# Optimization experiments

Hardware: AMD Instinct MI355X
Metric: run time of the kernel (lower is better)

## Reference

```python
import jax, jax.numpy as jnp
import numpy as np

ALPHA = 0.2  # LeakyReLU negative slope
N_NODES = 50000
N_EDGES = 800000
IN_F = 128
OUT_F = 64


def setup_inputs() -> dict:
    key = jax.random.key(0)
    k1, k2, k3, k4 = jax.random.split(key, 4)
    x = jax.random.normal(k1, (N_NODES, IN_F), dtype=jnp.float32)
    edge_index = jax.random.randint(k2, (2, N_EDGES), 0, N_NODES, dtype=jnp.int64)
    # xavier_uniform-ish scales
    W = jax.random.uniform(k3, (IN_F, OUT_F), dtype=jnp.float32,
                           minval=-1.0, maxval=1.0) * (1.414 * np.sqrt(6.0 / (IN_F + OUT_F)))
    a = jax.random.uniform(k4, (2 * OUT_F, 1), dtype=jnp.float32,
                           minval=-1.0, maxval=1.0) * (1.414 * np.sqrt(6.0 / (2 * OUT_F + 1)))
    return {"x": x, "edge_index": edge_index, "W": W, "a": a}


def reference(x, edge_index, W, a):
    Wh = x @ W                               # [N, F_out]
    src = edge_index[0]
    dst = edge_index[1]
    Wh_src = Wh[src]                         # [E, F_out] gather
    Wh_dst = Wh[dst]                         # [E, F_out] gather
    # concat([Wh_src, Wh_dst]) @ a == Wh_src @ a_top + Wh_dst @ a_bot
    F_out = Wh.shape[1]
    a_top = a[:F_out, 0]
    a_bot = a[F_out:, 0]
    e = jax.nn.leaky_relu(Wh_src @ a_top + Wh_dst @ a_bot, negative_slope=ALPHA)  # [E]
    # NOTE: original normalizes softmax over ALL edges (dim=0), not per node.
    attention = jax.nn.softmax(e)            # [E]
    # dropout skipped (eval mode, deterministic reference)
    msgs = Wh_dst * attention[:, None]       # [E, F_out]
    h_prime = jax.ops.segment_sum(msgs, src, num_segments=Wh.shape[0])  # scatter-add
    return jax.nn.elu(h_prime)
```

## Files before the change

### kernel.cpp

```cpp
#include <hip/hip_runtime.h>
#include <math.h>

#define N_NODES 50000
#define N_EDGES 800000
#define IN_F 128
#define OUT_F 64
#define LRELU_ALPHA 0.2f

#define NPB 128
#define NBUCK ((N_NODES + NPB - 1) / NPB)
#define EPT 8
#define NBT ((N_EDGES / EPT + 255) / 256)
#define CHUNK 2048

typedef __attribute__((ext_vector_type(8))) short bf16x8;
typedef __attribute__((ext_vector_type(4))) float f32x4;

__device__ inline float wred_max(float v) {
#pragma unroll
    for (int o = 32; o > 0; o >>= 1) v = fmaxf(v, __shfl_down(v, o, 64));
    return v;
}
__device__ inline float wred_sum(float v) {
#pragma unroll
    for (int o = 32; o > 0; o >>= 1) v += __shfl_down(v, o, 64);
    return v;
}

__device__ inline unsigned bf16r(float f) {
    unsigned u = __float_as_uint(f);
    u += 0x7fffu + ((u >> 16) & 1u);
    return u >> 16;
}

__global__ __launch_bounds__(128) void k_proj(const float* __restrict__ W,
                                              const float* __restrict__ a,
                                              float* __restrict__ wt,
                                              float* __restrict__ wb,
                                              unsigned short* __restrict__ Wtb) {
    int k = threadIdx.x;
    float s = 0.0f, t = 0.0f;
#pragma unroll
    for (int c4 = 0; c4 < 64; c4 += 4) {
        float4 wv = *reinterpret_cast<const float4*>(W + k * 64 + c4);
        float4 at = *reinterpret_cast<const float4*>(a + c4);
        float4 ab = *reinterpret_cast<const float4*>(a + 64 + c4);
        s = fmaf(wv.w, at.w, fmaf(wv.z, at.z, fmaf(wv.y, at.y, fmaf(wv.x, at.x, s))));
        t = fmaf(wv.w, ab.w, fmaf(wv.z, ab.z, fmaf(wv.y, ab.y, fmaf(wv.x, ab.x, t))));
        Wtb[(c4 + 0) * 128 + k] = (unsigned short)bf16r(wv.x);
        Wtb[(c4 + 1) * 128 + k] = (unsigned short)bf16r(wv.y);
        Wtb[(c4 + 2) * 128 + k] = (unsigned short)bf16r(wv.z);
        Wtb[(c4 + 3) * 128 + k] = (unsigned short)bf16r(wv.w);
    }
    wt[k] = s;
    wb[k] = t;
}

__global__ __launch_bounds__(256, 4) void k_wh(const float* __restrict__ x,
                                               const unsigned short* __restrict__ Wtb,
                                               const float* __restrict__ wt,
                                               const float* __restrict__ wb,
                                               const int* __restrict__ src,
                                               unsigned short* __restrict__ Whb,
                                               float* __restrict__ sv,
                                               float* __restrict__ tv,
                                               int* __restrict__ bcnt) {
    __shared__ unsigned short xb[64 * 128];
    __shared__ unsigned short wtl[64 * 128];
    __shared__ int hc[NBUCK];

    const int tid = threadIdx.x;
    const int row0 = blockIdx.x * 64;

    for (int i = tid; i < NBUCK; i += 256) hc[i] = 0;

    for (int ci = tid; ci < 1024; ci += 256) {
        int c = ci >> 4, kb = ci & 15;
        int4 v = *reinterpret_cast<const int4*>(Wtb + ci * 8);
        *reinterpret_cast<int4*>(&wtl[c * 128 + (kb ^ (c & 15)) * 8]) = v;
    }

    const int cc = (tid & 31) << 2;
    float4 wt4 = *reinterpret_cast<const float4*>(wt + cc);
    float4 wb4 = *reinterpret_cast<const float4*>(wb + cc);
    float ps[8], pt[8];
#pragma unroll
    for (int it = 0; it < 8; ++it) {
        int i = tid + it * 256;
        int rl = i >> 5;
        int r = row0 + rl;
        float4 v = make_float4(0.f, 0.f, 0.f, 0.f);
        if (r < N_NODES) v = *reinterpret_cast<const float4*>(x + (size_t)r * IN_F + cc);
        ps[it] = fmaf(v.w, wt4.w, fmaf(v.z, wt4.z, fmaf(v.y, wt4.y, v.x * wt4.x)));
        pt[it] = fmaf(v.w, wb4.w, fmaf(v.z, wb4.z, fmaf(v.y, wb4.y, v.x * wb4.x)));
        int kb = cc >> 3;
        uint2 pk;
        pk.x = bf16r(v.x) | (bf16r(v.y) << 16);
        pk.y = bf16r(v.z) | (bf16r(v.w) << 16);
        *reinterpret_cast<uint2*>(
            &xb[rl * 128 + (kb ^ (rl & 15)) * 8 + ((cc >> 2) & 1) * 4]) = pk;
    }

    {
        int j0 = blockIdx.x * 1024 + tid * 4;
        if (j0 < N_EDGES) {
            int4 s4 = *reinterpret_cast<const int4*>(src + j0);
            atomicAdd(&hc[s4.x >> 7], 1);
            atomicAdd(&hc[s4.y >> 7], 1);
            atomicAdd(&hc[s4.z >> 7], 1);
            atomicAdd(&hc[s4.w >> 7], 1);
        }
    }
    __syncthreads();

    const int l = tid & 63, w = tid >> 6;
    const int rloc0 = w * 16;
    const int arow = rloc0 + (l & 15);
    const int kgrp = l >> 4;
    f32x4 acc[4] = {f32x4{0,0,0,0}, f32x4{0,0,0,0}, f32x4{0,0,0,0}, f32x4{0,0,0,0}};
#pragma unroll
    for (int t = 0; t < 4; ++t) {
        int kb = t * 4 + kgrp;
        bf16x8 af = *reinterpret_cast<const bf16x8*>(
            &xb[arow * 128 + (kb ^ (arow & 15)) * 8]);
#pragma unroll
        for (int ct = 0; ct < 4; ++ct) {
            int brow = ct * 16 + (l & 15);
            bf16x8 bfr = *reinterpret_cast<const bf16x8*>(
                &wtl[brow * 128 + (kb ^ (brow & 15)) * 8]);
            acc[ct] = __builtin_amdgcn_mfma_f32_16x16x32_bf16(af, bfr, acc[ct], 0, 0, 0);
        }
    }

#pragma unroll
    for (int ct = 0; ct < 4; ++ct) {
#pragma unroll
        for (int i = 0; i < 4; ++i) {
            int r = row0 + rloc0 + (l >> 4) * 4 + i;
            if (r < N_NODES)
                Whb[(size_t)r * OUT_F + ct * 16 + (l & 15)] =
                    (unsigned short)bf16r(acc[ct][i]);
        }
    }

#pragma unroll
    for (int it = 0; it < 8; ++it) {
        float s = ps[it], t2 = pt[it];
#pragma unroll
        for (int o = 1; o < 32; o <<= 1) {
            s += __shfl_xor(s, o, 64);
            t2 += __shfl_xor(t2, o, 64);
        }
        int r = row0 + (tid >> 5) + it * 8;
        if ((tid & 31) == 0 && r < N_NODES) { sv[r] = s; tv[r] = t2; }
    }

    __syncthreads();
    for (int i = tid; i < NBUCK; i += 256) {
        int v = hc[i];
        if (v) atomicAdd(&bcnt[i], v);
    }
}

__global__ __launch_bounds__(512) void k_bscan(const int* __restrict__ bcnt,
                                               int* __restrict__ bbase,
                                               int* __restrict__ cursor) {
    __shared__ int s[512];
    int t = threadIdx.x;
    int c = (t < NBUCK) ? bcnt[t] : 0;
    s[t] = c;
    __syncthreads();
#pragma unroll
    for (int o = 1; o < 512; o <<= 1) {
        int v = (t >= o) ? s[t - o] : 0;
        __syncthreads();
        s[t] += v;
        __syncthreads();
    }
    if (t < NBUCK) {
        int ex = s[t] - c;
        bbase[t] = ex;
        cursor[t] = ex;
    }
    if (t == 0) bbase[NBUCK] = N_EDGES;
}

__global__ __launch_bounds__(256) void k_binscatter(const int* __restrict__ src,
                                                    const int* __restrict__ dst,
                                                    const float* __restrict__ sv,
                                                    const float* __restrict__ tv,
                                                    int* __restrict__ cursor,
                                                    int2* __restrict__ rec,
                                                    float* __restrict__ pmax,
                                                    float* __restrict__ psum) {
    __shared__ int lcnt[NBUCK];
    __shared__ int lbase[NBUCK];
    const int tid = threadIdx.x;
    for (int i = tid; i < NBUCK; i += 256) lcnt[i] = 0;
    __syncthreads();

    int t = blockIdx.x * 256 + tid;
    int j0 = t * EPT;
    bool ok = (j0 < N_EDGES);

    int s_[EPT], d_[EPT], rk[EPT];
    float v[EPT];
    float lmax = -INFINITY;
    if (ok) {
        int4 a4 = *reinterpret_cast<const int4*>(src + j0);
        int4 b4 = *reinterpret_cast<const int4*>(src + j0 + 4);
        int4 c4 = *reinterpret_cast<const int4*>(dst + j0);
        int4 e4 = *reinterpret_cast<const int4*>(dst + j0 + 4);
        s_[0] = a4.x; s_[1] = a4.y; s_[2] = a4.z; s_[3] = a4.w;
        s_[4] = b4.x; s_[5] = b4.y; s_[6] = b4.z; s_[7] = b4.w;
        d_[0] = c4.x; d_[1] = c4.y; d_[2] = c4.z; d_[3] = c4.w;
        d_[4] = e4.x; d_[5] = e4.y; d_[6] = e4.z; d_[7] = e4.w;
        float svv[EPT], tvv[EPT];
#pragma unroll
        for (int k = 0; k < EPT; k++) svv[k] = sv[s_[k]];
#pragma unroll
        for (int k = 0; k < EPT; k++) tvv[k] = tv[d_[k]];
#pragma unroll
        for (int k = 0; k < EPT; k++) {
            float vv = svv[k] + tvv[k];
            vv = vv > 0.0f ? vv : LRELU_ALPHA * vv;
            v[k] = vv;
            lmax = fmaxf(lmax, vv);
        }
#pragma unroll
        for (int k = 0; k < EPT; k++) rk[k] = atomicAdd(&lcnt[s_[k] >> 7], 1);
    }
    __syncthreads();

    for (int i = tid; i < NBUCK; i += 256) {
        int c = lcnt[i];
        lbase[i] = c ? atomicAdd(&cursor[i], c) : 0;
    }
    __syncthreads();

    if (ok) {
#pragma unroll
        for (int k = 0; k < EPT; k++) {
            int b = s_[k] >> 7;
            rec[lbase[b] + rk[k]] =
                make_int2(d_[k] | ((s_[k] & (NPB - 1)) << 16), __float_as_int(v[k]));
        }
    }

    float wm = wred_max(lmax);
    wm = __shfl(wm, 0, 64);
    float ev = 0.0f;
    if (ok) {
#pragma unroll
        for (int k = 0; k < EPT; k++) ev += __expf(v[k] - wm);
    }
    float wsum = wred_sum(ev);

    __shared__ float rmx[4], rsm[4];
    if ((tid & 63) == 0) {
        rmx[tid >> 6] = wm;
        rsm[tid >> 6] = wsum;
    }
    __syncthreads();
    if (tid == 0) {
        float bm = fmaxf(fmaxf(rmx[0], rmx[1]), fmaxf(rmx[2], rmx[3]));
        float bs = 0.0f;
#pragma unroll
        for (int i = 0; i < 4; i++)
            bs += (rmx[i] == -INFINITY) ? 0.0f : rsm[i] * __expf(rmx[i] - bm);
        pmax[blockIdx.x] = bm;
        psum[blockIdx.x] = bs;
    }
}

__global__ __launch_bounds__(1024) void k_rcombine(const float* __restrict__ pmax,
                                                   const float* __restrict__ psum,
                                                   int n, float* __restrict__ g) {
    __shared__ float red[16];
    __shared__ float gm_s;
    int t = threadIdx.x;
    float lmax = -INFINITY;
    for (int i = t; i < n; i += 1024) lmax = fmaxf(lmax, pmax[i]);
    float wm = wred_max(lmax);
    if ((t & 63) == 0) red[t >> 6] = wm;
    __syncthreads();
    if (t == 0) {
        float m = red[0];
        for (int i = 1; i < 16; i++) m = fmaxf(m, red[i]);
        gm_s = m;
    }
    __syncthreads();
    float gm = gm_s;
    float lsum = 0.0f;
    for (int i = t; i < n; i += 1024)
        lsum += (pmax[i] == -INFINITY) ? 0.0f : psum[i] * __expf(pmax[i] - gm);
    float ws = wred_sum(lsum);
    __syncthreads();
    if ((t & 63) == 0) red[t >> 6] = ws;
    __syncthreads();
    if (t == 0) {
        float s = 0.0f;
        for (int i = 0; i < 16; i++) s += red[i];
        g[0] = gm;
        g[1] = 1.0f / s;
    }
}

__global__ __launch_bounds__(1024) void k_bgather(const int* __restrict__ bbase,
                                                  const int2* __restrict__ rec,
                                                  const float* __restrict__ g,
                                                  const unsigned short* __restrict__ Whb,
                                                  float* __restrict__ out) {
    __shared__ int2 sorted[CHUNK];
    __shared__ int scnt[NPB], soff[NPB], shead[NPB];

    const int tid = threadIdx.x;
    const int lane = tid & 63, w = tid >> 6;
    const int j = lane & 31, h = lane >> 5;
    const int b = blockIdx.x;
    const float gm = g[0], ginv = g[1];
    const int e0 = bbase[b], e1 = bbase[b + 1];

    float ax[8], ay[8];
#pragma unroll
    for (int k = 0; k < 8; k++) { ax[k] = 0.0f; ay[k] = 0.0f; }

    for (int base = e0; base < e1; base += CHUNK) {
        int m = e1 - base;
        if (m > CHUNK) m = CHUNK;

        bool va = (tid < m), vb = (tid + 1024 < m);
        int2 ra = make_int2(0, 0), rb = make_int2(0, 0);
        int lna = 0, lnb = 0;
        if (tid < NPB) scnt[tid] = 0;
        __syncthreads();
        if (va) {
            ra = rec[base + tid];
            lna = (ra.x >> 16) & (NPB - 1);
            atomicAdd(&scnt[lna], 1);
        }
        if (vb) {
            rb = rec[base + tid + 1024];
            lnb = (rb.x >> 16) & (NPB - 1);
            atomicAdd(&scnt[lnb], 1);
        }
        __syncthreads();

        if (tid < 64) {
            int c0 = scnt[2 * tid], c1 = scnt[2 * tid + 1];
            int s = c0 + c1;
            int run = s;
#pragma unroll
            for (int o = 1; o < 64; o <<= 1) {
                int src_ln = (tid >= o) ? (tid - o) : tid;
                int t2 = __shfl(run, src_ln, 64);
                if (tid >= o) run += t2;
            }
            int excl = run - s;
            soff[2 * tid] = excl;
            soff[2 * tid + 1] = excl + c0;
            shead[2 * tid] = excl;
            shead[2 * tid + 1] = excl + c0;
        }
        __syncthreads();

        if (va) {
            int pos = atomicAdd(&shead[lna], 1);
            sorted[pos] = make_int2(ra.x & 0xFFFF, ra.y);
        }
        if (vb) {
            int pos = atomicAdd(&shead[lnb], 1);
            sorted[pos] = make_int2(rb.x & 0xFFFF, rb.y);
        }
        __syncthreads();

#pragma unroll
        for (int k = 0; k < 8; k++) {
            int node = w * 8 + k;
            int lo = soff[node], c = scnt[node];
            float px = 0.0f, py = 0.0f;
            int i = 0;
            for (; i + 7 < c; i += 8) {
                int2 q0 = sorted[lo + i + h];
                int2 q1 = sorted[lo + i + 2 + h];
                int2 q2 = sorted[lo + i + 4 + h];
                int2 q3 = sorted[lo + i + 6 + h];
                const unsigned* p0 =
                    reinterpret_cast<const unsigned*>(Whb + (size_t)q0.x * OUT_F);
                const unsigned* p1 =
                    reinterpret_cast<const unsigned*>(Whb + (size_t)q1.x * OUT_F);
                const unsigned* p2 =
                    reinterpret_cast<const unsigned*>(Whb + (size_t)q2.x * OUT_F);
                const unsigned* p3 =
                    reinterpret_cast<const unsigned*>(Whb + (size_t)q3.x * OUT_F);
                unsigned u0 = p0[j];
                unsigned u1 = p1[j];
                unsigned u2 = p2[j];
                unsigned u3 = p3[j];
                float att0 = __expf(__int_as_float(q0.y) - gm);
                float att1 = __expf(__int_as_float(q1.y) - gm);
                float att2 = __expf(__int_as_float(q2.y) - gm);
                float att3 = __expf(__int_as_float(q3.y) - gm);
                px = fmaf(att0, __uint_as_float((u0 & 0xffffu) << 16), px);
                py = fmaf(att0, __uint_as_float(u0 & 0xffff0000u), py);
                px = fmaf(att1, __uint_as_float((u1 & 0xffffu) << 16), px);
                py = fmaf(att1, __uint_as_float(u1 & 0xffff0000u), py);
                px = fmaf(att2, __uint_as_float((u2 & 0xffffu) << 16), px);
                py = fmaf(att2, __uint_as_float(u2 & 0xffff0000u), py);
                px = fmaf(att3, __uint_as_float((u3 & 0xffffu) << 16), px);
                py = fmaf(att3, __uint_as_float(u3 & 0xffff0000u), py);
            }
            for (; i < c; i += 2) {
                int ii = i + h;
                bool val = ii < c;
                int2 q = sorted[lo + (val ? ii : i)];
                const unsigned* p =
                    reinterpret_cast<const unsigned*>(Whb + (size_t)q.x * OUT_F);
                unsigned u = p[j];
                float att = val ? __expf(__int_as_float(q.y) - gm) : 0.0f;
                px = fmaf(att, __uint_as_float((u & 0xffffu) << 16), px);
                py = fmaf(att, __uint_as_float(u & 0xffff0000u), py);
            }
            ax[k] += px;
            ay[k] += py;
        }
        __syncthreads();
    }

#pragma unroll
    for (int k = 0; k < 8; k++) {
        float sx = ax[k] + __shfl_down(ax[k], 32, 64);
        float sy = ay[k] + __shfl_down(ay[k], 32, 64);
        int n = b * NPB + w * 8 + k;
        if (h == 0 && n < N_NODES) {
            float2 v;
            v.x = sx * ginv;
            v.y = sy * ginv;
            v.x = v.x > 0.0f ? v.x : expm1f(v.x);
            v.y = v.y > 0.0f ? v.y : expm1f(v.y);
            *reinterpret_cast<float2*>(out + (size_t)n * OUT_F + 2 * j) = v;
        }
    }
}

extern "C" void kernel_launch(void* const* d_in, const int* in_sizes, int n_in,
                              void* d_out, int out_size, void* d_ws, size_t ws_size,
                              hipStream_t stream) {
    const float* x  = (const float*)d_in[0];
    const int*   ei = (const int*)d_in[1];
    const float* W  = (const float*)d_in[2];
    const float* a  = (const float*)d_in[3];
    float* out = (float*)d_out;

    const int* src = ei;
    const int* dst = ei + N_EDGES;

    unsigned short* Whb = (unsigned short*)d_ws;
    float* sv     = (float*)(Whb + (size_t)N_NODES * OUT_F);
    float* tv     = sv + N_NODES;
    float* pmax   = tv + N_NODES;
    float* psum   = pmax + 512;
    float* g      = psum + 512;
    float* wt     = g + 2;
    float* wb     = wt + 128;
    int*   bcnt   = (int*)(wb + 128);
    int*   bbase  = bcnt + NBUCK;
    int*   cursor = bbase + NBUCK + 1;
    size_t used = (size_t)((char*)(cursor + NBUCK) - (char*)d_ws);
    used = (used + 15) & ~(size_t)15;
    unsigned short* Wtb = (unsigned short*)((char*)d_ws + used);
    used += 8192 * sizeof(unsigned short);
    used = (used + 15) & ~(size_t)15;
    int2*  rec  = (int2*)((char*)d_ws + used);

    hipMemsetAsync(bcnt, 0, NBUCK * sizeof(int), stream);
    k_proj<<<1, 128, 0, stream>>>(W, a, wt, wb, Wtb);
    k_wh<<<(N_NODES + 63) / 64, 256, 0, stream>>>(x, Wtb, wt, wb, src, Whb, sv, tv, bcnt);
    k_bscan<<<1, 512, 0, stream>>>(bcnt, bbase, cursor);
    k_binscatter<<<NBT, 256, 0, stream>>>(src, dst, sv, tv, cursor, rec, pmax, psum);
    k_rcombine<<<1, 1024, 0, stream>>>(pmax, psum, NBT, g);
    k_bgather<<<NBUCK, 1024, 0, stream>>>(bbase, rec, g, Whb, out);
}
```

Measured before the change: 118.2 us.

## Halve bucket size to 64 nodes and use 512-thread gather blocks; fold memset

Source nodes are now binned into buckets of 64 instead of 128, which doubles the bucket count to 782, so the gather kernel launches more, smaller blocks of 512 threads that each load up to four records per chunk. The histogram, bin-scatter, scan (now 1024 threads) and gather prefix-sum are adjusted to match. The separate memset of the bucket counters is folded into the projection kernel, which removes one launch. The aim is better occupancy and load balance across CUs in the gather phase, at the cost of more atomic targets and more buckets to scan.

```diff
diff --git a/kernel.cpp b/kernel.cpp
--- a/kernel.cpp
+++ b/kernel.cpp
@@ -7,7 +7,7 @@
 #define OUT_F 64
 #define LRELU_ALPHA 0.2f
 
-#define NPB 128
+#define NPB 64
 #define NBUCK ((N_NODES + NPB - 1) / NPB)
 #define EPT 8
 #define NBT ((N_EDGES / EPT + 255) / 256)
@@ -33,12 +33,15 @@
     return u >> 16;
 }
 
-__global__ __launch_bounds__(128) void k_proj(const float* __restrict__ W,
-                                              const float* __restrict__ a,
-                                              float* __restrict__ wt,
-                                              float* __restrict__ wb,
-                                              unsigned short* __restrict__ Wtb) {
+__global__ __launch_bounds__(1024) void k_proj(const float* __restrict__ W,
+                                               const float* __restrict__ a,
+                                               float* __restrict__ wt,
+                                               float* __restrict__ wb,
+                                               unsigned short* __restrict__ Wtb,
+                                               int* __restrict__ bcnt) {
     int k = threadIdx.x;
+    if (k < NBUCK) bcnt[k] = 0;
+    if (k >= 128) return;
     float s = 0.0f, t = 0.0f;
 #pragma unroll
     for (int c4 = 0; c4 < 64; c4 += 4) {
@@ -105,10 +108,10 @@
         int j0 = blockIdx.x * 1024 + tid * 4;
         if (j0 < N_EDGES) {
             int4 s4 = *reinterpret_cast<const int4*>(src + j0);
-            atomicAdd(&hc[s4.x >> 7], 1);
-            atomicAdd(&hc[s4.y >> 7], 1);
-            atomicAdd(&hc[s4.z >> 7], 1);
-            atomicAdd(&hc[s4.w >> 7], 1);
+            atomicAdd(&hc[s4.x >> 6], 1);
+            atomicAdd(&hc[s4.y >> 6], 1);
+            atomicAdd(&hc[s4.z >> 6], 1);
+            atomicAdd(&hc[s4.w >> 6], 1);
         }
     }
     __syncthreads();
@@ -162,16 +165,16 @@
     }
 }
 
-__global__ __launch_bounds__(512) void k_bscan(const int* __restrict__ bcnt,
-                                               int* __restrict__ bbase,
-                                               int* __restrict__ cursor) {
-    __shared__ int s[512];
+__global__ __launch_bounds__(1024) void k_bscan(const int* __restrict__ bcnt,
+                                                int* __restrict__ bbase,
+                                                int* __restrict__ cursor) {
+    __shared__ int s[1024];
     int t = threadIdx.x;
     int c = (t < NBUCK) ? bcnt[t] : 0;
     s[t] = c;
     __syncthreads();
 #pragma unroll
-    for (int o = 1; o < 512; o <<= 1) {
+    for (int o = 1; o < 1024; o <<= 1) {
         int v = (t >= o) ? s[t - o] : 0;
         __syncthreads();
         s[t] += v;
@@ -228,7 +231,7 @@
             lmax = fmaxf(lmax, vv);
         }
 #pragma unroll
-        for (int k = 0; k < EPT; k++) rk[k] = atomicAdd(&lcnt[s_[k] >> 7], 1);
+        for (int k = 0; k < EPT; k++) rk[k] = atomicAdd(&lcnt[s_[k] >> 6], 1);
     }
     __syncthreads();
 
@@ -241,7 +244,7 @@
     if (ok) {
 #pragma unroll
         for (int k = 0; k < EPT; k++) {
-            int b = s_[k] >> 7;
+            int b = s_[k] >> 6;
             rec[lbase[b] + rk[k]] =
                 make_int2(d_[k] | ((s_[k] & (NPB - 1)) << 16), __float_as_int(v[k]));
         }
@@ -306,11 +309,11 @@
     }
 }
 
-__global__ __launch_bounds__(1024) void k_bgather(const int* __restrict__ bbase,
-                                                  const int2* __restrict__ rec,
-                                                  const float* __restrict__ g,
-                                                  const unsigned short* __restrict__ Whb,
-                                                  float* __restrict__ out) {
+__global__ __launch_bounds__(512) void k_bgather(const int* __restrict__ bbase,
+                                                 const int2* __restrict__ rec,
+                                                 const float* __restrict__ g,
+                                                 const unsigned short* __restrict__ Whb,
+                                                 float* __restrict__ out) {
     __shared__ int2 sorted[CHUNK];
     __shared__ int scnt[NPB], soff[NPB], shead[NPB];
 
@@ -329,48 +332,46 @@
         int m = e1 - base;
         if (m > CHUNK) m = CHUNK;
 
-        bool va = (tid < m), vb = (tid + 1024 < m);
-        int2 ra = make_int2(0, 0), rb = make_int2(0, 0);
-        int lna = 0, lnb = 0;
+        int2 rr[4];
+        int ln[4];
+        bool vv[4];
         if (tid < NPB) scnt[tid] = 0;
         __syncthreads();
-        if (va) {
-            ra = rec[base + tid];
-            lna = (ra.x >> 16) & (NPB - 1);
-            atomicAdd(&scnt[lna], 1);
-        }
-        if (vb) {
-            rb = rec[base + tid + 1024];
-            lnb = (rb.x >> 16) & (NPB - 1);
-            atomicAdd(&scnt[lnb], 1);
+#pragma unroll
+        for (int q = 0; q < 4; q++) {
+            int idx = tid + q * 512;
+            vv[q] = idx < m;
+            rr[q] = make_int2(0, 0);
+            ln[q] = 0;
+            if (vv[q]) {
+                rr[q] = rec[base + idx];
+                ln[q] = (rr[q].x >> 16) & (NPB - 1);
+                atomicAdd(&scnt[ln[q]], 1);
+            }
         }
         __syncthreads();
 
         if (tid < 64) {
-            int c0 = scnt[2 * tid], c1 = scnt[2 * tid + 1];
-            int s = c0 + c1;
-            int run = s;
+            int c = scnt[tid];
+            int run = c;
 #pragma unroll
             for (int o = 1; o < 64; o <<= 1) {
                 int src_ln = (tid >= o) ? (tid - o) : tid;
                 int t2 = __shfl(run, src_ln, 64);
                 if (tid >= o) run += t2;
             }
-            int excl = run - s;
-            soff[2 * tid] = excl;
-            soff[2 * tid + 1] = excl + c0;
-            shead[2 * tid] = excl;
-            shead[2 * tid + 1] = excl + c0;
-        }
-        __syncthreads();
-
-        if (va) {
-            int pos = atomicAdd(&shead[lna], 1);
-            sorted[pos] = make_int2(ra.x & 0xFFFF, ra.y);
-        }
-        if (vb) {
-            int pos = atomicAdd(&shead[lnb], 1);
-            sorted[pos] = make_int2(rb.x & 0xFFFF, rb.y);
+            int excl = run - c;
+            soff[tid] = excl;
+            shead[tid] = excl;
+        }
+        __syncthreads();
+
+#pragma unroll
+        for (int q = 0; q < 4; q++) {
+            if (vv[q]) {
+                int pos = atomicAdd(&shead[ln[q]], 1);
+                sorted[pos] = make_int2(rr[q].x & 0xFFFF, rr[q].y);
+            }
         }
         __syncthreads();
 
@@ -473,11 +474,10 @@
     used = (used + 15) & ~(size_t)15;
     int2*  rec  = (int2*)((char*)d_ws + used);
 
-    hipMemsetAsync(bcnt, 0, NBUCK * sizeof(int), stream);
-    k_proj<<<1, 128, 0, stream>>>(W, a, wt, wb, Wtb);
+    k_proj<<<1, 1024, 0, stream>>>(W, a, wt, wb, Wtb, bcnt);
     k_wh<<<(N_NODES + 63) / 64, 256, 0, stream>>>(x, Wtb, wt, wb, src, Whb, sv, tv, bcnt);
-    k_bscan<<<1, 512, 0, stream>>>(bcnt, bbase, cursor);
+    k_bscan<<<1, 1024, 0, stream>>>(bcnt, bbase, cursor);
     k_binscatter<<<NBT, 256, 0, stream>>>(src, dst, sv, tv, cursor, rec, pmax, psum);
     k_rcombine<<<1, 1024, 0, stream>>>(pmax, psum, NBT, g);
-    k_bgather<<<NBUCK, 1024, 0, stream>>>(bbase, rec, g, Whb, out);
-}
+    k_bgather<<<NBUCK, 512, 0, stream>>>(bbase, rec, g, Whb, out);
+}
```

After: 106.4 us. -10.0%, faster.
